# Optimization experiments

Hardware: AMD Instinct MI355X
Metric: run time of the kernel (lower is better)

## Reference

```python
import jax, jax.numpy as jnp
import numpy as np

B, S, E, H, NQ, FF = 2, 2048, 768, 12, 8, 3072
DK = E // H
EPS = 1e-5


def _layernorm(x, g, b):
    m = jnp.mean(x, axis=-1, keepdims=True)
    v = jnp.mean((x - m) ** 2, axis=-1, keepdims=True)
    return (x - m) * jax.lax.rsqrt(v + EPS) * g + b


def setup_inputs() -> dict:
    key = jax.random.key(0)
    ks = jax.random.split(key, 12)
    s = 0.02
    return {
        'x': jax.random.normal(ks[0], (B, S, E), dtype=jnp.float32),
        'W_o': jax.random.normal(ks[1], (E, E), dtype=jnp.float32) * s,
        'b_o': jnp.zeros((E,), dtype=jnp.float32),
        'g1': jnp.ones((E,), dtype=jnp.float32),
        'be1': jnp.zeros((E,), dtype=jnp.float32),
        'g2': jnp.ones((E,), dtype=jnp.float32),
        'be2': jnp.zeros((E,), dtype=jnp.float32),
        'ry': jax.random.normal(ks[2], (NQ,), dtype=jnp.float32),
        'W1': jax.random.normal(ks[3], (NQ, FF), dtype=jnp.float32) * s,
        'b1': jnp.zeros((FF,), dtype=jnp.float32),
        'W2': jax.random.normal(ks[4], (FF, E), dtype=jnp.float32) * s,
        'b2': jnp.zeros((E,), dtype=jnp.float32),
    }


def reference(x, W_o, b_o, g1, be1, g2, be2, ry, W1, b1, W2, b2):
    # --- multi-head self-attention (q = k = v = x, no QKV projection) ---
    q = x.reshape(B, S, H, DK).transpose(0, 2, 1, 3)  # [B,H,S,DK]
    scores = jnp.einsum('bhqd,bhkd->bhqk', q, q) / jnp.sqrt(jnp.float32(DK))
    attn = jax.nn.softmax(scores, axis=-1)
    out = jnp.einsum('bhqk,bhkd->bhqd', attn, q)
    out = out.transpose(0, 2, 1, 3).reshape(B, S, E)
    attn_out = out @ W_o + b_o

    x = _layernorm(x + attn_out, g1, be1)

    # --- quantum FFN: per-wire RX(x_i) encode, RY(ry_i), <Z> = cos(x_i)*cos(ry_i) ---
    q_meas = jnp.cos(x[..., :NQ]) * jnp.cos(ry)  # [B,S,NQ]
    ffn_out = jax.nn.relu(q_meas @ W1 + b1) @ W2 + b2

    return _layernorm(x + ffn_out, g2, be2)
```

## Files before the change

kernel.cpp:

```cpp
#include <hip/hip_runtime.h>
#include <hip/hip_bf16.h>

#define B_  2
#define S_  2048
#define E_  768
#define H_  12
#define DK_ 64
#define NQ_ 8
#define FF_ 3072
#define EPS_ 1e-5f

typedef __attribute__((ext_vector_type(8))) short short8;
typedef __attribute__((ext_vector_type(4))) float f32x4;
typedef __hip_bfloat16 bf16;

__device__ __forceinline__ bf16 f2bh(float f) { return __float2bfloat16(f); }
__device__ __forceinline__ short f2b(float f) {
    bf16 h = __float2bfloat16(f);
    return *reinterpret_cast<short*>(&h);
}

__device__ __forceinline__ int swz(int row, int col) {
    return (col & 7) | ((((col >> 3) ^ (row & 7)) & 7) << 3);
}

__device__ __forceinline__ f32x4 mfma16(short8 a, short8 b, f32x4 c) {
    return __builtin_amdgcn_mfma_f32_16x16x32_bf16(a, b, c, 0, 0, 0);
}

__global__ __launch_bounds__(256) void prep_cvt(const float* __restrict__ x,
                                                bf16* __restrict__ xb, int n4) {
    int i = blockIdx.x * 256 + threadIdx.x;
    if (i >= n4) return;
    float4 f = *(const float4*)(x + (size_t)i * 4);
    short4 sv;
    sv.x = f2b(f.x); sv.y = f2b(f.y); sv.z = f2b(f.z); sv.w = f2b(f.w);
    *(short4*)((short*)xb + (size_t)i * 4) = sv;
}

__global__ __launch_bounds__(256) void transpose_cvt(const float* __restrict__ W,
                                                     bf16* __restrict__ WT,
                                                     int K, int N) {
    __shared__ float tile[32][33];
    int k0 = blockIdx.y * 32, n0 = blockIdx.x * 32;
    int tx = threadIdx.x & 31, ty = threadIdx.x >> 5;
#pragma unroll
    for (int i = 0; i < 4; i++) {
        int row = ty + i * 8;
        tile[row][tx] = W[(size_t)(k0 + row) * N + n0 + tx];
    }
    __syncthreads();
#pragma unroll
    for (int i = 0; i < 4; i++) {
        int row = ty + i * 8;
        WT[(size_t)(n0 + row) * K + k0 + tx] = f2bh(tile[tx][row]);
    }
}

__global__ __launch_bounds__(256) void prep_w1t(const float* __restrict__ W1,
                                                bf16* __restrict__ W1bT) {
    int k = blockIdx.x * 256 + threadIdx.x;
    if (k >= FF_) return;
    short8 v;
#pragma unroll
    for (int i = 0; i < NQ_; i++) v[i] = f2b(W1[(size_t)i * FF_ + k]);
    *(short8*)(W1bT + (size_t)k * NQ_) = v;
}

__global__ __launch_bounds__(256) void attn_kernel(const bf16* __restrict__ xb,
                                                   bf16* __restrict__ out) {
    const int qtiles = S_ / 64;
    const int nwg = B_ * H_ * qtiles;
    int o = blockIdx.x;
    int blk = (o & 7) * (nwg >> 3) + (o >> 3);
    int qt = blk % qtiles;
    int hh = (blk / qtiles) % H_;
    int bb = blk / (qtiles * H_);
    const bf16* base = xb + (size_t)bb * S_ * E_ + hh * DK_;

    __shared__ __align__(16) bf16 Ks[64][64];
    __shared__ __align__(16) bf16 Vt[64][64];
    __shared__ __align__(16) bf16 Pl[4][16][64];

    int t = threadIdx.x;
    int w = t >> 6, l = t & 63, c = l & 15, g = l >> 4;

    short8 qf[2];
    {
        const bf16* qp = base + (size_t)(qt * 64 + w * 16 + c) * E_;
        qf[0] = *(const short8*)(qp + g * 8);
        qf[1] = *(const short8*)(qp + 32 + g * 8);
    }

    f32x4 oacc[4];
    float l_part[4];
#pragma unroll
    for (int n = 0; n < 4; n++) { oacc[n] = (f32x4){0.f, 0.f, 0.f, 0.f}; l_part[n] = 0.f; }

    int skey = t & 63;
    int scb0 = t >> 6;

    short8 pre[2];
#pragma unroll
    for (int it = 0; it < 2; it++)
        pre[it] = *(const short8*)(base + (size_t)skey * E_ + (scb0 + it * 4) * 8);

    for (int kt = 0; kt < S_ / 64; kt++) {
#pragma unroll
        for (int it = 0; it < 2; it++) {
            int cb = scb0 + it * 4;
            *(short8*)&Ks[skey][swz(skey, cb * 8)] = pre[it];
#pragma unroll
            for (int j = 0; j < 8; j++) {
                int d = cb * 8 + j;
                short sv = pre[it][j];
                Vt[d][swz(d, skey)] = *reinterpret_cast<bf16*>(&sv);
            }
        }
        __syncthreads();

        if (kt + 1 < S_ / 64) {
#pragma unroll
            for (int it = 0; it < 2; it++)
                pre[it] = *(const short8*)(base + (size_t)((kt + 1) * 64 + skey) * E_ + (scb0 + it * 4) * 8);
        }

        f32x4 sfr[4];
#pragma unroll
        for (int n = 0; n < 4; n++) {
            sfr[n] = (f32x4){0.f, 0.f, 0.f, 0.f};
#pragma unroll
            for (int kh = 0; kh < 2; kh++) {
                const short8 bfr = *(const short8*)&Ks[n * 16 + c][swz(n * 16 + c, kh * 32 + g * 8)];
                sfr[n] = mfma16(qf[kh], bfr, sfr[n]);
            }
        }
#pragma unroll
        for (int jj = 0; jj < 4; jj++) {
            float pv[4];
#pragma unroll
            for (int n = 0; n < 4; n++)
                pv[n] = exp2f(sfr[n][jj] * 0.18033688f);
            l_part[jj] += (pv[0] + pv[1]) + (pv[2] + pv[3]);
            int r = g * 4 + jj;
#pragma unroll
            for (int n = 0; n < 4; n++)
                Pl[w][r][swz(r, n * 16 + c)] = f2bh(pv[n]);
        }

#pragma unroll
        for (int ks = 0; ks < 2; ks++) {
            short8 vb[4];
#pragma unroll
            for (int dn = 0; dn < 4; dn++)
                vb[dn] = *(const short8*)&Vt[dn * 16 + c][swz(dn * 16 + c, ks * 32 + g * 8)];
            const short8 pa = *(const short8*)&Pl[w][c][swz(c, ks * 32 + g * 8)];
#pragma unroll
            for (int dn = 0; dn < 4; dn++)
                oacc[dn] = mfma16(pa, vb[dn], oacc[dn]);
        }
        __syncthreads();
    }

#pragma unroll
    for (int jj = 0; jj < 4; jj++) {
        float lv = l_part[jj];
#pragma unroll
        for (int msk = 1; msk < 16; msk <<= 1) lv += __shfl_xor(lv, msk);
        float inv = 1.f / lv;
        size_t ro = ((size_t)bb * S_ + qt * 64 + w * 16 + g * 4 + jj) * E_ + hh * DK_;
#pragma unroll
        for (int dn = 0; dn < 4; dn++)
            out[ro + dn * 16 + c] = f2bh(oacc[dn][jj] * inv);
    }
}

__global__ __launch_bounds__(256) void gemm_bf16(const bf16* __restrict__ A,
                                                 const bf16* __restrict__ BT,
                                                 const float* __restrict__ bias,
                                                 bf16* __restrict__ C,
                                                 int M, int N, int K) {
    __shared__ __align__(16) bf16 As2[2][64][64];
    __shared__ __align__(16) bf16 Bs2[2][64][64];
    int nbx = gridDim.x, nwg = nbx * gridDim.y;
    int id = blockIdx.y * nbx + blockIdx.x;
    int id2 = (nwg & 7) ? id : ((id & 7) * (nwg >> 3) + (id >> 3));
    int row0 = (id2 / nbx) * 64, col0 = (id2 % nbx) * 64;
    int t = threadIdx.x, w = t >> 6, l = t & 63, c = l & 15, g = l >> 4;

    f32x4 acc[4];
#pragma unroll
    for (int n = 0; n < 4; n++) acc[n] = (f32x4){0.f, 0.f, 0.f, 0.f};

    int srow = t & 63, scb = t >> 6;
    const bf16* ap = A + (size_t)(row0 + srow) * K;
    const bf16* bp = BT + (size_t)(col0 + srow) * K;

    short8 pA0, pA1, pB0, pB1;
    pA0 = *(const short8*)(ap + scb * 8);
    pA1 = *(const short8*)(ap + (scb + 4) * 8);
    pB0 = *(const short8*)(bp + scb * 8);
    pB1 = *(const short8*)(bp + (scb + 4) * 8);
    *(short8*)&As2[0][srow][swz(srow, scb * 8)] = pA0;
    *(short8*)&As2[0][srow][swz(srow, (scb + 4) * 8)] = pA1;
    *(short8*)&Bs2[0][srow][swz(srow, scb * 8)] = pB0;
    *(short8*)&Bs2[0][srow][swz(srow, (scb + 4) * 8)] = pB1;
    if (64 < K) {
        pA0 = *(const short8*)(ap + 64 + scb * 8);
        pA1 = *(const short8*)(ap + 64 + (scb + 4) * 8);
        pB0 = *(const short8*)(bp + 64 + scb * 8);
        pB1 = *(const short8*)(bp + 64 + (scb + 4) * 8);
    }
    __syncthreads();

    int cur = 0;
    for (int k0 = 0; k0 < K; k0 += 64, cur ^= 1) {
        int nxt = cur ^ 1;
        if (k0 + 64 < K) {
            *(short8*)&As2[nxt][srow][swz(srow, scb * 8)] = pA0;
            *(short8*)&As2[nxt][srow][swz(srow, (scb + 4) * 8)] = pA1;
            *(short8*)&Bs2[nxt][srow][swz(srow, scb * 8)] = pB0;
            *(short8*)&Bs2[nxt][srow][swz(srow, (scb + 4) * 8)] = pB1;
        }
        if (k0 + 128 < K) {
            pA0 = *(const short8*)(ap + k0 + 128 + scb * 8);
            pA1 = *(const short8*)(ap + k0 + 128 + (scb + 4) * 8);
            pB0 = *(const short8*)(bp + k0 + 128 + scb * 8);
            pB1 = *(const short8*)(bp + k0 + 128 + (scb + 4) * 8);
        }
#pragma unroll
        for (int kh = 0; kh < 2; kh++) {
            const short8 af = *(const short8*)&As2[cur][w * 16 + c][swz(w * 16 + c, kh * 32 + g * 8)];
#pragma unroll
            for (int n = 0; n < 4; n++) {
                const short8 bfr = *(const short8*)&Bs2[cur][n * 16 + c][swz(n * 16 + c, kh * 32 + g * 8)];
                acc[n] = mfma16(af, bfr, acc[n]);
            }
        }
        __syncthreads();
    }
#pragma unroll
    for (int jj = 0; jj < 4; jj++) {
        int row = row0 + w * 16 + g * 4 + jj;
#pragma unroll
        for (int n = 0; n < 4; n++) {
            int col = col0 + n * 16 + c;
            C[(size_t)row * N + col] = f2bh(acc[n][jj] + bias[col]);
        }
    }
}

__global__ __launch_bounds__(256) void gemm2_mfma(const float* __restrict__ xln,
                                                  const float* __restrict__ ry,
                                                  const bf16* __restrict__ W1bT,
                                                  const float* __restrict__ b1,
                                                  const bf16* __restrict__ W2bT,
                                                  const float* __restrict__ b2,
                                                  bf16* __restrict__ C) {
    __shared__ __align__(16) bf16 As[64][64];
    __shared__ __align__(16) bf16 Bs[2][64][64];
    __shared__ __align__(16) bf16 W1t[2][64][8];
    __shared__ __align__(16) bf16 qm_s[64][8];
    const int nbx = E_ / 64;
    const int nwg = nbx * (B_ * S_ / 64);
    int id = blockIdx.y * nbx + blockIdx.x;
    int id2 = (id & 7) * (nwg >> 3) + (id >> 3);
    int row0 = (id2 / nbx) * 64, col0 = (id2 % nbx) * 64;
    int t = threadIdx.x, w = t >> 6, l = t & 63, c = l & 15, g = l >> 4;

    if (t < 64) {
        const float* xp = xln + (size_t)(row0 + t) * E_;
#pragma unroll
        for (int i = 0; i < NQ_; i++)
            qm_s[t][i] = f2bh(cosf(xp[i]) * cosf(ry[i]));
    }

    f32x4 acc[4];
#pragma unroll
    for (int n = 0; n < 4; n++) acc[n] = (f32x4){0.f, 0.f, 0.f, 0.f};

    int srow = t & 63, scb = t >> 6;
    const bf16* brow_p = W2bT + (size_t)(col0 + srow) * FF_;

    short8 preB0, preB1, preW;
    preB0 = *(const short8*)(brow_p + scb * 8);
    preB1 = *(const short8*)(brow_p + (scb + 4) * 8);
    if (t < 64) preW = *(const short8*)(W1bT + (size_t)t * NQ_);
    *(short8*)&Bs[0][srow][swz(srow, scb * 8)] = preB0;
    *(short8*)&Bs[0][srow][swz(srow, (scb + 4) * 8)] = preB1;
    if (t < 64) *(short8*)&W1t[0][t][0] = preW;
    preB0 = *(const short8*)(brow_p + 64 + scb * 8);
    preB1 = *(const short8*)(brow_p + 64 + (scb + 4) * 8);
    if (t < 64) preW = *(const short8*)(W1bT + (size_t)(64 + t) * NQ_);
    __syncthreads();

    short8 zz = {0, 0, 0, 0, 0, 0, 0, 0};
    short8 aq = zz;
    if (g == 0) aq = *(const short8*)&qm_s[w * 16 + c][0];

    int cur = 0;
    for (int k0 = 0; k0 < FF_; k0 += 64, cur ^= 1) {
        float b1c[4];
#pragma unroll
        for (int n = 0; n < 4; n++) b1c[n] = b1[k0 + n * 16 + c];

        int nxt = cur ^ 1;
        if (k0 + 64 < FF_) {
            *(short8*)&Bs[nxt][srow][swz(srow, scb * 8)] = preB0;
            *(short8*)&Bs[nxt][srow][swz(srow, (scb + 4) * 8)] = preB1;
            if (t < 64) *(short8*)&W1t[nxt][t][0] = preW;
        }
        if (k0 + 128 < FF_) {
            preB0 = *(const short8*)(brow_p + k0 + 128 + scb * 8);
            preB1 = *(const short8*)(brow_p + k0 + 128 + (scb + 4) * 8);
            if (t < 64) preW = *(const short8*)(W1bT + (size_t)(k0 + 128 + t) * NQ_);
        }

        f32x4 zero4 = {0.f, 0.f, 0.f, 0.f};
#pragma unroll
        for (int n = 0; n < 4; n++) {
            short8 bw = zz;
            if (g == 0) bw = *(const short8*)&W1t[cur][n * 16 + c][0];
            f32x4 hfr = mfma16(aq, bw, zero4);
#pragma unroll
            for (int jj = 0; jj < 4; jj++) {
                float hv = fmaxf(hfr[jj] + b1c[n], 0.f);
                int r = w * 16 + g * 4 + jj;
                As[r][swz(r, n * 16 + c)] = f2bh(hv);
            }
        }

#pragma unroll
        for (int kh = 0; kh < 2; kh++) {
            const short8 af = *(const short8*)&As[w * 16 + c][swz(w * 16 + c, kh * 32 + g * 8)];
#pragma unroll
            for (int n = 0; n < 4; n++) {
                const short8 bfr = *(const short8*)&Bs[cur][n * 16 + c][swz(n * 16 + c, kh * 32 + g * 8)];
                acc[n] = mfma16(af, bfr, acc[n]);
            }
        }
        __syncthreads();
    }
#pragma unroll
    for (int jj = 0; jj < 4; jj++) {
        int row = row0 + w * 16 + g * 4 + jj;
#pragma unroll
        for (int n = 0; n < 4; n++) {
            int col = col0 + n * 16 + c;
            C[(size_t)row * E_ + col] = f2bh(acc[n][jj] + b2[col]);
        }
    }
}

__global__ __launch_bounds__(256) void gemm2_fused(const float* __restrict__ xln,
                                                   const float* __restrict__ ry,
                                                   const float* __restrict__ W1,
                                                   const float* __restrict__ b1,
                                                   const float* __restrict__ W2,
                                                   const float* __restrict__ b2,
                                                   bf16* __restrict__ C) {
    __shared__ __align__(16) bf16 As[64][64];
    __shared__ __align__(16) bf16 Bst[64][64];
    __shared__ float qmS[64][NQ_];
    int row0 = blockIdx.y * 64, col0 = blockIdx.x * 64;
    int t = threadIdx.x, w = t >> 6, l = t & 63, c = l & 15, g = l >> 4;

    for (int idx = t; idx < 64 * NQ_; idx += 256) {
        int r = idx >> 3, i = idx & 7;
        qmS[r][i] = cosf(xln[(size_t)(row0 + r) * E_ + i]) * cosf(ry[i]);
    }

    f32x4 acc[4];
#pragma unroll
    for (int n = 0; n < 4; n++) acc[n] = (f32x4){0.f, 0.f, 0.f, 0.f};

    int kl = t & 63, rg = (t >> 6) * 16;
    int brow = t >> 4, bcol = (t & 15) * 4;

    for (int k0 = 0; k0 < FF_; k0 += 64) {
        __syncthreads();
        {
            float w1v[NQ_];
#pragma unroll
            for (int i = 0; i < NQ_; i++) w1v[i] = W1[i * FF_ + k0 + kl];
            float b1v = b1[k0 + kl];
#pragma unroll
            for (int r16 = 0; r16 < 16; r16++) {
                int r = rg + r16;
                float sh = b1v;
#pragma unroll
                for (int i = 0; i < NQ_; i++) sh += qmS[r][i] * w1v[i];
                As[r][swz(r, kl)] = f2bh(fmaxf(sh, 0.f));
            }
        }
#pragma unroll
        for (int it = 0; it < 4; it++) {
            int kk = brow + it * 16;
            float4 v = *(const float4*)(W2 + (size_t)(k0 + kk) * E_ + col0 + bcol);
            Bst[bcol + 0][swz(bcol + 0, kk)] = f2bh(v.x);
            Bst[bcol + 1][swz(bcol + 1, kk)] = f2bh(v.y);
            Bst[bcol + 2][swz(bcol + 2, kk)] = f2bh(v.z);
            Bst[bcol + 3][swz(bcol + 3, kk)] = f2bh(v.w);
        }
        __syncthreads();
#pragma unroll
        for (int kh = 0; kh < 2; kh++) {
            const short8 af = *(const short8*)&As[w * 16 + c][swz(w * 16 + c, kh * 32 + g * 8)];
#pragma unroll
            for (int n = 0; n < 4; n++) {
                const short8 bfr = *(const short8*)&Bst[n * 16 + c][swz(n * 16 + c, kh * 32 + g * 8)];
                acc[n] = mfma16(af, bfr, acc[n]);
            }
        }
    }
#pragma unroll
    for (int jj = 0; jj < 4; jj++) {
        int row = row0 + w * 16 + g * 4 + jj;
#pragma unroll
        for (int n = 0; n < 4; n++) {
            int col = col0 + n * 16 + c;
            C[(size_t)row * E_ + col] = f2bh(acc[n][jj] + b2[col]);
        }
    }
}

__global__ __launch_bounds__(256) void ln_add_b(const float* __restrict__ X,
                                                const bf16* __restrict__ Yb,
                                                const float* __restrict__ g,
                                                const float* __restrict__ be,
                                                float* __restrict__ out) {
    int r = blockIdx.x;
    const size_t off = (size_t)r * E_;
    int t = threadIdx.x;
    float v[3];
    float s = 0.f, s2 = 0.f;
#pragma unroll
    for (int j = 0; j < 3; j++) {
        int e = t + j * 256;
        float val = X[off + e] + __bfloat162float(Yb[off + e]);
        v[j] = val; s += val; s2 += val * val;
    }
#pragma unroll
    for (int msk = 32; msk > 0; msk >>= 1) {
        s += __shfl_xor(s, msk);
        s2 += __shfl_xor(s2, msk);
    }
    __shared__ float red[8];
    int lane = t & 63, wv = t >> 6;
    if (lane == 0) { red[wv] = s; red[4 + wv] = s2; }
    __syncthreads();
    if (t == 0) {
        red[0] = red[0] + red[1] + red[2] + red[3];
        red[4] = red[4] + red[5] + red[6] + red[7];
    }
    __syncthreads();
    float mean = red[0] * (1.f / E_);
    float var = red[4] * (1.f / E_) - mean * mean;
    float inv = rsqrtf(var + EPS_);
#pragma unroll
    for (int j = 0; j < 3; j++) {
        int e = t + j * 256;
        out[off + e] = (v[j] - mean) * inv * g[e] + be[e];
    }
}

extern "C" void kernel_launch(void* const* d_in, const int* in_sizes, int n_in,
                              void* d_out, int out_size, void* d_ws, size_t ws_size,
                              hipStream_t stream) {
    const float* x   = (const float*)d_in[0];
    const float* W_o = (const float*)d_in[1];
    const float* b_o = (const float*)d_in[2];
    const float* g1  = (const float*)d_in[3];
    const float* be1 = (const float*)d_in[4];
    const float* g2  = (const float*)d_in[5];
    const float* be2 = (const float*)d_in[6];
    const float* ry  = (const float*)d_in[7];
    const float* W1  = (const float*)d_in[8];
    const float* b1  = (const float*)d_in[9];
    const float* W2  = (const float*)d_in[10];
    const float* b2  = (const float*)d_in[11];
    float* out = (float*)d_out;

    const size_t BSE = (size_t)B_ * S_ * E_;
    char* ws = (char*)d_ws;

    const size_t FAST_NEED = 37404672;
    bool fast = ws_size >= FAST_NEED;

    bf16* xb    = (bf16*)(ws + 0);
    bf16* attnb = (bf16*)(ws + 6291456);
    bf16* WobT  = fast ? (bf16*)(ws + 12582912) : (bf16*)(ws + 18874368);
    bf16* W2bT  = (bf16*)(ws + 13762560);
    bf16* tmp1b = fast ? (bf16*)(ws + 18481152) : (bf16*)(ws + 12582912);
    float* xln  = (float*)(ws + (fast ? 24772608 : 20054016));
    bf16* W1bT  = (bf16*)(ws + 37355520);
    bf16* tmp2b = tmp1b;

    prep_cvt<<<dim3((BSE / 4 + 255) / 256), 256, 0, stream>>>(x, xb, BSE / 4);
    transpose_cvt<<<dim3(E_ / 32, E_ / 32), 256, 0, stream>>>(W_o, WobT, E_, E_);
    if (fast) {
        transpose_cvt<<<dim3(E_ / 32, FF_ / 32), 256, 0, stream>>>(W2, W2bT, FF_, E_);
        prep_w1t<<<dim3(FF_ / 256), 256, 0, stream>>>(W1, W1bT);
    }

    attn_kernel<<<dim3(B_ * H_ * (S_ / 64)), 256, 0, stream>>>(xb, attnb);
    gemm_bf16<<<dim3(E_ / 64, (B_ * S_) / 64), 256, 0, stream>>>(
        attnb, WobT, b_o, tmp1b, B_ * S_, E_, E_);
    ln_add_b<<<dim3(B_ * S_), 256, 0, stream>>>(x, tmp1b, g1, be1, xln);

    if (fast) {
        gemm2_mfma<<<dim3(E_ / 64, (B_ * S_) / 64), 256, 0, stream>>>(
            xln, ry, W1bT, b1, W2bT, b2, tmp2b);
    } else {
        gemm2_fused<<<dim3(E_ / 64, (B_ * S_) / 64), 256, 0, stream>>>(
            xln, ry, W1, b1, W2, b2, tmp2b);
    }
    ln_add_b<<<dim3(B_ * S_), 256, 0, stream>>>(xln, tmp2b, g2, be2, out);
}
```

Measured before the change: 178.7 us.

## Precompute transposed bf16 x for attention V tiles and raise MFMA priority

Adds a prep kernel that writes both the bf16 copy of x and a per-batch transposed bf16 copy, so the attention kernel can load V tiles already transposed with vector stores instead of scattering eight scalar LDS writes per element. It also wraps the MFMA sections in s_setprio to favour matrix instructions across waves. The cost is an extra 6 MB workspace buffer, more global reads per key tile in attention, and a fast path that is only taken when the workspace is larger.

```diff
diff --git a/kernel.cpp b/kernel.cpp
--- a/kernel.cpp
+++ b/kernel.cpp
@@ -28,6 +28,28 @@
     return __builtin_amdgcn_mfma_f32_16x16x32_bf16(a, b, c, 0, 0, 0);
 }
 
+__global__ __launch_bounds__(256) void prep_xall(const float* __restrict__ x,
+                                                 bf16* __restrict__ xb,
+                                                 bf16* __restrict__ xT) {
+    __shared__ float tile[32][33];
+    int e0 = blockIdx.x * 32, s0 = blockIdx.y * 32;
+    int tx = threadIdx.x & 31, ty = threadIdx.x >> 5;
+    int b = s0 >> 11, sl0 = s0 & 2047;
+#pragma unroll
+    for (int i = 0; i < 4; i++) {
+        int row = ty + i * 8;
+        float v = x[(size_t)(s0 + row) * E_ + e0 + tx];
+        tile[row][tx] = v;
+        xb[(size_t)(s0 + row) * E_ + e0 + tx] = f2bh(v);
+    }
+    __syncthreads();
+#pragma unroll
+    for (int i = 0; i < 4; i++) {
+        int row = ty + i * 8;
+        xT[((size_t)b * E_ + e0 + row) * S_ + sl0 + tx] = f2bh(tile[tx][row]);
+    }
+}
+
 __global__ __launch_bounds__(256) void prep_cvt(const float* __restrict__ x,
                                                 bf16* __restrict__ xb, int n4) {
     int i = blockIdx.x * 256 + threadIdx.x;
@@ -67,7 +89,9 @@
     *(short8*)(W1bT + (size_t)k * NQ_) = v;
 }
 
+template<bool XT>
 __global__ __launch_bounds__(256) void attn_kernel(const bf16* __restrict__ xb,
+                                                   const bf16* __restrict__ xT,
                                                    bf16* __restrict__ out) {
     const int qtiles = S_ / 64;
     const int nwg = B_ * H_ * qtiles;
@@ -77,6 +101,7 @@
     int hh = (blk / qtiles) % H_;
     int bb = blk / (qtiles * H_);
     const bf16* base = xb + (size_t)bb * S_ * E_ + hh * DK_;
+    const bf16* baseT = xT + ((size_t)bb * E_ + hh * DK_) * S_;
 
     __shared__ __align__(16) bf16 Ks[64][64];
     __shared__ __align__(16) bf16 Vt[64][64];
@@ -100,32 +125,43 @@
     int skey = t & 63;
     int scb0 = t >> 6;
 
-    short8 pre[2];
-#pragma unroll
-    for (int it = 0; it < 2; it++)
-        pre[it] = *(const short8*)(base + (size_t)skey * E_ + (scb0 + it * 4) * 8);
+    short8 preK[2], preV[2];
+#pragma unroll
+    for (int it = 0; it < 2; it++) {
+        preK[it] = *(const short8*)(base + (size_t)skey * E_ + (scb0 + it * 4) * 8);
+        if (XT)
+            preV[it] = *(const short8*)(baseT + (size_t)skey * S_ + (scb0 + it * 4) * 8);
+    }
 
     for (int kt = 0; kt < S_ / 64; kt++) {
 #pragma unroll
         for (int it = 0; it < 2; it++) {
             int cb = scb0 + it * 4;
-            *(short8*)&Ks[skey][swz(skey, cb * 8)] = pre[it];
-#pragma unroll
-            for (int j = 0; j < 8; j++) {
-                int d = cb * 8 + j;
-                short sv = pre[it][j];
-                Vt[d][swz(d, skey)] = *reinterpret_cast<bf16*>(&sv);
+            *(short8*)&Ks[skey][swz(skey, cb * 8)] = preK[it];
+            if (XT) {
+                *(short8*)&Vt[skey][swz(skey, cb * 8)] = preV[it];
+            } else {
+#pragma unroll
+                for (int j = 0; j < 8; j++) {
+                    int d = cb * 8 + j;
+                    short sv = preK[it][j];
+                    Vt[d][swz(d, skey)] = *reinterpret_cast<bf16*>(&sv);
+                }
             }
         }
         __syncthreads();
 
         if (kt + 1 < S_ / 64) {
 #pragma unroll
-            for (int it = 0; it < 2; it++)
-                pre[it] = *(const short8*)(base + (size_t)((kt + 1) * 64 + skey) * E_ + (scb0 + it * 4) * 8);
+            for (int it = 0; it < 2; it++) {
+                preK[it] = *(const short8*)(base + (size_t)((kt + 1) * 64 + skey) * E_ + (scb0 + it * 4) * 8);
+                if (XT)
+                    preV[it] = *(const short8*)(baseT + (size_t)skey * S_ + (kt + 1) * 64 + (scb0 + it * 4) * 8);
+            }
         }
 
         f32x4 sfr[4];
+        __builtin_amdgcn_s_setprio(1);
 #pragma unroll
         for (int n = 0; n < 4; n++) {
             sfr[n] = (f32x4){0.f, 0.f, 0.f, 0.f};
@@ -135,6 +171,7 @@
                 sfr[n] = mfma16(qf[kh], bfr, sfr[n]);
             }
         }
+        __builtin_amdgcn_s_setprio(0);
 #pragma unroll
         for (int jj = 0; jj < 4; jj++) {
             float pv[4];
@@ -148,6 +185,7 @@
                 Pl[w][r][swz(r, n * 16 + c)] = f2bh(pv[n]);
         }
 
+        __builtin_amdgcn_s_setprio(1);
 #pragma unroll
         for (int ks = 0; ks < 2; ks++) {
             short8 vb[4];
@@ -159,6 +197,7 @@
             for (int dn = 0; dn < 4; dn++)
                 oacc[dn] = mfma16(pa, vb[dn], oacc[dn]);
         }
+        __builtin_amdgcn_s_setprio(0);
         __syncthreads();
     }
 
@@ -484,7 +523,7 @@
     const size_t BSE = (size_t)B_ * S_ * E_;
     char* ws = (char*)d_ws;
 
-    const size_t FAST_NEED = 37404672;
+    const size_t FAST_NEED = 43696128;
     bool fast = ws_size >= FAST_NEED;
 
     bf16* xb    = (bf16*)(ws + 0);
@@ -494,16 +533,23 @@
     bf16* tmp1b = fast ? (bf16*)(ws + 18481152) : (bf16*)(ws + 12582912);
     float* xln  = (float*)(ws + (fast ? 24772608 : 20054016));
     bf16* W1bT  = (bf16*)(ws + 37355520);
+    bf16* xT    = (bf16*)(ws + 37404672);
     bf16* tmp2b = tmp1b;
 
-    prep_cvt<<<dim3((BSE / 4 + 255) / 256), 256, 0, stream>>>(x, xb, BSE / 4);
-    transpose_cvt<<<dim3(E_ / 32, E_ / 32), 256, 0, stream>>>(W_o, WobT, E_, E_);
     if (fast) {
+        prep_xall<<<dim3(E_ / 32, B_ * S_ / 32), 256, 0, stream>>>(x, xb, xT);
         transpose_cvt<<<dim3(E_ / 32, FF_ / 32), 256, 0, stream>>>(W2, W2bT, FF_, E_);
         prep_w1t<<<dim3(FF_ / 256), 256, 0, stream>>>(W1, W1bT);
-    }
-
-    attn_kernel<<<dim3(B_ * H_ * (S_ / 64)), 256, 0, stream>>>(xb, attnb);
+    } else {
+        prep_cvt<<<dim3((int)((BSE / 4 + 255) / 256)), 256, 0, stream>>>(x, xb, (int)(BSE / 4));
+    }
+    transpose_cvt<<<dim3(E_ / 32, E_ / 32), 256, 0, stream>>>(W_o, WobT, E_, E_);
+
+    if (fast)
+        attn_kernel<true><<<dim3(B_ * H_ * (S_ / 64)), 256, 0, stream>>>(xb, xT, attnb);
+    else
+        attn_kernel<false><<<dim3(B_ * H_ * (S_ / 64)), 256, 0, stream>>>(xb, xb, attnb);
+
     gemm_bf16<<<dim3(E_ / 64, (B_ * S_) / 64), 256, 0, stream>>>(
         attnb, WobT, b_o, tmp1b, B_ * S_, E_, E_);
     ln_add_b<<<dim3(B_ * S_), 256, 0, stream>>>(x, tmp1b, g1, be1, xln);
```

Result: faster. 174.6 us (-2.3%).
